# Kernel optimization log

Hardware: AMD Instinct MI355X
Metric: run time of the kernel (lower is better)

The kernel has to match this reference:

```python
import jax, jax.numpy as jnp
import numpy as np

N = 50000   # nodes
E = 400000  # edges
D = 128     # hidden = out dim
H = 4       # heads
DH = 32     # head dim (D // H)
T = 3       # node types
R = 6       # relation (edge) types
L = 2       # layers
EPS = 1e-5


def setup_inputs() -> dict:
    key = jax.random.key(0)
    ks = jax.random.split(key, 12)
    s = D ** -0.5
    sh = DH ** -0.5
    return {
        "h": jax.random.normal(ks[0], (N, D), jnp.float32),
        "src": jax.random.randint(ks[1], (E,), 0, N),
        "dst": jax.random.randint(ks[2], (E,), 0, N),
        "ntype": jnp.sort(jax.random.randint(ks[3], (N,), 0, T)),
        "etype": jnp.sort(jax.random.randint(ks[4], (E,), 0, R)),
        # per-layer HGTConv params (stacked over L)
        "Wk": jax.random.normal(ks[5], (L, T, D, D), jnp.float32) * s,
        "Wq": jax.random.normal(ks[6], (L, T, D, D), jnp.float32) * s,
        "Wv": jax.random.normal(ks[7], (L, T, D, D), jnp.float32) * s,
        "Wa": jax.random.normal(ks[8], (L, T, D, D), jnp.float32) * s,
        "W_att": jax.random.normal(ks[9], (L, H, R, DH, DH), jnp.float32) * sh,
        "W_msg": jax.random.normal(ks[10], (L, H, R, DH, DH), jnp.float32) * sh,
        "pri": jnp.ones((L, H, R), jnp.float32),
        "skip": jnp.ones((L, T), jnp.float32),
        "ln_g": jnp.ones((L, D), jnp.float32),
        "ln_b": jnp.zeros((L, D), jnp.float32),
        # LayerAggregator params
        "agg_w": jnp.ones((L,), jnp.float32),
        "agg_g": jnp.ones((D,), jnp.float32),
        "agg_b": jnp.zeros((D,), jnp.float32),
    }


def typed_linear(x, types, W):
    # W: [T, in, out]; per-node-type linear (DGL TypedLinear, no bias)
    out = x @ W[0]
    for t in range(1, W.shape[0]):
        out = jnp.where((types == t)[:, None], x @ W[t], out)
    return out


def edge_typed(x, etype, W):
    # x: [E, H, DH]; W: [H, R, DH, DH]; per-relation, per-head linear
    out = jnp.einsum('ehd,hdo->eho', x, W[:, 0])
    for r in range(1, W.shape[1]):
        out = jnp.where((etype == r)[:, None, None],
                        jnp.einsum('ehd,hdo->eho', x, W[:, r]), out)
    return out


def layer_norm(x, g, b):
    mu = x.mean(-1, keepdims=True)
    var = ((x - mu) ** 2).mean(-1, keepdims=True)
    return (x - mu) * jax.lax.rsqrt(var + EPS) * g + b


def hgt_layer(x, src, dst, ntype, etype, Wk, Wq, Wv, Wa, W_att, W_msg, pri, skip):
    n = x.shape[0]
    k = typed_linear(x, ntype, Wk).reshape(n, H, DH)
    q = typed_linear(x, ntype, Wq).reshape(n, H, DH)
    v = typed_linear(x, ntype, Wv).reshape(n, H, DH)
    kw = edge_typed(k[src], etype, W_att)          # [E,H,DH]
    mv = edge_typed(v[src], etype, W_msg)          # [E,H,DH]
    a = (kw * q[dst]).sum(-1) * pri.T[etype] / np.sqrt(DH).astype(np.float32)  # [E,H]
    # edge softmax over destination nodes
    mx = jax.lax.stop_gradient(jax.ops.segment_max(a, dst, num_segments=n))
    ex = jnp.exp(a - mx[dst])
    den = jax.ops.segment_sum(ex, dst, num_segments=n)
    att = ex / den[dst]                             # [E,H]
    agg = jax.ops.segment_sum(att[:, :, None] * mv, dst, num_segments=n)
    h_a = typed_linear(agg.reshape(n, H * DH), ntype, Wa)
    sk = jax.nn.sigmoid(skip)[ntype][:, None]
    return h_a * sk + x * (1.0 - sk)                # skip gate (dropout = eval identity)


def reference(h, src, dst, ntype, etype, Wk, Wq, Wv, Wa, W_att, W_msg,
              pri, skip, ln_g, ln_b, agg_w, agg_g, agg_b):
    x = h
    outs = []
    for l in range(L):
        ho = hgt_layer(x, src, dst, ntype, etype, Wk[l], Wq[l], Wv[l], Wa[l],
                       W_att[l], W_msg[l], pri[l], skip[l])
        # residual is Identity (in_dim == out_dim), dropout is eval-mode identity
        x = layer_norm(x + ho, ln_g[l], ln_b[l])
        outs.append(x)
    w = jax.nn.softmax(agg_w)
    mixed = sum(w[i] * outs[i] for i in range(L))
    return layer_norm(mixed, agg_g, agg_b)  # [N, D]; per-type dict is just slicing by ntype
```

## Files before the change

kernel.cpp:

```cpp
#include <hip/hip_runtime.h>

#define NN 50000
#define NE 400000
#define DD 128
#define HH 4
#define DHH 32
#define TT 3
#define RR 6
#define LL 2
#define EPSF 1e-5f

typedef unsigned short ushort_t;
typedef unsigned int uint_t;
typedef __attribute__((ext_vector_type(8))) short short8_t;
typedef __attribute__((ext_vector_type(4))) float float4_t;

__device__ inline ushort_t f2bf(float f){
  union { float f; uint_t u; } x; x.f = f;
  uint_t r = x.u + 0x7fffu + ((x.u >> 16) & 1u);
  return (ushort_t)(r >> 16);
}
__device__ inline float bf2f(ushort_t u){
  union { uint_t u; float f; } x; x.u = ((uint_t)u) << 16;
  return x.f;
}
__device__ inline uint_t pack2(float a, float b){
  return (uint_t)f2bf(a) | ((uint_t)f2bf(b) << 16);
}

__global__ void hist_kernel(const int* __restrict__ dst, int* __restrict__ cnt){
  int e = blockIdx.x*256 + threadIdx.x;
  if (e < NE) atomicAdd(&cnt[dst[e]], 1);
}

__global__ void scan_kernel(const int* __restrict__ deg, int* __restrict__ rowptr){
  __shared__ int wsum[16];
  __shared__ int carrySh;
  int tid = threadIdx.x, lane = tid & 63, w = tid >> 6;
  if (tid == 0){ carrySh = 0; rowptr[0] = 0; }
  __syncthreads();
  for (int base = 0; base < NN; base += 1024){
    int i = base + tid;
    int v = (i < NN) ? deg[i] : 0;
    int s = v;
    #pragma unroll
    for (int off=1; off<64; off<<=1){ int t = __shfl_up(s, off); if (lane >= off) s += t; }
    if (lane == 63) wsum[w] = s;
    __syncthreads();
    if (w == 0 && lane < 16){
      int t = wsum[lane];
      #pragma unroll
      for (int off=1; off<16; off<<=1){ int u = __shfl_up(t, off); if (lane >= off) t += u; }
      wsum[lane] = t;
    }
    __syncthreads();
    int waveOff = (w == 0) ? 0 : wsum[w-1];
    int incl = s + waveOff + carrySh;
    if (i < NN) rowptr[i+1] = incl;
    __syncthreads();
    if (tid == 0) carrySh += wsum[15];
    __syncthreads();
  }
}

__global__ void scatter_kernel(const int* __restrict__ dst, const int* __restrict__ src,
                               const int* __restrict__ etype, const int* __restrict__ rowptr,
                               int* __restrict__ cnt, uint_t* __restrict__ sr){
  int e = blockIdx.x*256 + threadIdx.x;
  if (e < NE){
    int d = dst[e];
    int pos = rowptr[d] + atomicAdd(&cnt[d], 1);
    sr[pos] = (uint_t)src[e] | ((uint_t)etype[e] << 27);
  }
}

__global__ void wprep_kernel(const float* __restrict__ Wk, const float* __restrict__ Wq,
                             const float* __restrict__ Wv, const float* __restrict__ Wa,
                             ushort_t* __restrict__ Wkf, ushort_t* __restrict__ Wqf,
                             ushort_t* __restrict__ Wvf, ushort_t* __restrict__ Waf){
  int i = blockIdx.x*256 + threadIdx.x;
  if (i < TT*DD*DD){
    int j = i & 7, m = (i>>3)&15, kg = (i>>7)&3, ks = (i>>9)&3, tile = (i>>11)&7, t = i>>14;
    int d = ks*32 + kg*4 + (j&3) + ((j>>2)<<4);
    int o = tile*16 + m;
    size_t srcI = (size_t)t*16384 + (size_t)d*DD + o;
    Wkf[i] = f2bf(Wk[srcI]);
    Wqf[i] = f2bf(Wq[srcI]);
    Wvf[i] = f2bf(Wv[srcI]);
    Waf[i] = f2bf(Wa[srcI]);
  }
}

__global__ void wprep2_kernel(const float* __restrict__ Watt, const float* __restrict__ Wmsg,
                              ushort_t* __restrict__ Wattf, ushort_t* __restrict__ Wmsgf){
  int i = blockIdx.x*256 + threadIdx.x;
  if (i < HH*RR*DHH*DHH){
    int j = i & 7, m = (i>>3)&15, kg = (i>>7)&3;
    int tile = (i>>9) % 12, h = i / 6144;
    int nout = tile*16 + m;
    int r = nout >> 5, dd = nout & 31;
    int k = kg*4 + (j&3) + ((j>>2)<<4);
    Wattf[i] = f2bf(Watt[(((h*RR + r)*DHH + dd)<<5) + k]);
    Wmsgf[i] = f2bf(Wmsg[(((h*RR + r)*DHH + k)<<5) + dd]);
  }
}

__global__ __launch_bounds__(256) void kqv_kernel(
    const float* __restrict__ x, const int* __restrict__ ntype,
    const float* __restrict__ Wk, const float* __restrict__ Wq, const float* __restrict__ Wv,
    const ushort_t* __restrict__ Wkf, const ushort_t* __restrict__ Wqf, const ushort_t* __restrict__ Wvf,
    const ushort_t* __restrict__ Wattf, const ushort_t* __restrict__ Wmsgf,
    const float* __restrict__ pri,
    ushort_t* __restrict__ kout, ushort_t* __restrict__ qh, ushort_t* __restrict__ vhat)
{
  __shared__ int nts[16];
  __shared__ ushort_t smem[24704];
  ushort_t* xs_ = smem;
  ushort_t* qs_ = smem + 2112;
  ushort_t* vs_ = smem + 4224;
  ushort_t* ks_ = smem + 6336;
  ushort_t* stg1 = smem;
  ushort_t* stg2 = smem + 12352;
  int tid = threadIdx.x;
  int n0 = blockIdx.x * 16;
  if (tid < 16) nts[tid] = ntype[n0 + tid];
  #pragma unroll
  for (int it=0; it<8; it++){
    int i = tid + it*256;
    xs_[(i>>7)*132 + (i&127)] = f2bf(x[(size_t)n0*DD + i]);
  }
  __syncthreads();
  int t0 = nts[0];
  bool uni = true;
  #pragma unroll
  for (int j=1;j<16;j++) uni = uni && (nts[j] == t0);

  int lane = tid & 63;
  union U8 { struct { uint2 lo, hi; } u; short8_t s; uint4 q; };

  if (uni){
    int w = tid >> 6;
    int m = lane & 15, kg = lane >> 4;
    float4_t acck0{0.f,0.f,0.f,0.f}, acck1{0.f,0.f,0.f,0.f};
    float4_t accq0{0.f,0.f,0.f,0.f}, accq1{0.f,0.f,0.f,0.f};
    float4_t accv0{0.f,0.f,0.f,0.f}, accv1{0.f,0.f,0.f,0.f};
    const ushort_t* wkf = Wkf + (size_t)t0*16384;
    const ushort_t* wqf = Wqf + (size_t)t0*16384;
    const ushort_t* wvf = Wvf + (size_t)t0*16384;
    int tA = 2*w, tB = 2*w+1;
    #pragma unroll
    for (int ks=0; ks<4; ks++){
      U8 a_;
      a_.u.lo = *(const uint2*)&xs_[m*132 + ks*32 + kg*4];
      a_.u.hi = *(const uint2*)&xs_[m*132 + ks*32 + kg*4 + 16];
      int offA = (((tA*4 + ks)*4 + kg) << 7) + (m << 3);
      int offB = (((tB*4 + ks)*4 + kg) << 7) + (m << 3);
      U8 bk0, bk1, bq0, bq1, bv0, bv1;
      bk0.q = *(const uint4*)(wkf + offA);
      bk1.q = *(const uint4*)(wkf + offB);
      bq0.q = *(const uint4*)(wqf + offA);
      bq1.q = *(const uint4*)(wqf + offB);
      bv0.q = *(const uint4*)(wvf + offA);
      bv1.q = *(const uint4*)(wvf + offB);
      acck0 = __builtin_amdgcn_mfma_f32_16x16x32_bf16(bk0.s, a_.s, acck0, 0,0,0);
      acck1 = __builtin_amdgcn_mfma_f32_16x16x32_bf16(bk1.s, a_.s, acck1, 0,0,0);
      accq0 = __builtin_amdgcn_mfma_f32_16x16x32_bf16(bq0.s, a_.s, accq0, 0,0,0);
      accq1 = __builtin_amdgcn_mfma_f32_16x16x32_bf16(bq1.s, a_.s, accq1, 0,0,0);
      accv0 = __builtin_amdgcn_mfma_f32_16x16x32_bf16(bv0.s, a_.s, accv0, 0,0,0);
      accv1 = __builtin_amdgcn_mfma_f32_16x16x32_bf16(bv1.s, a_.s, accv1, 0,0,0);
    }
    int cA = tA*16 + (kg<<2), cB = tB*16 + (kg<<2);
    *(uint2*)(&ks_[m*132 + cA]) = make_uint2(pack2(acck0[0],acck0[1]), pack2(acck0[2],acck0[3]));
    *(uint2*)(&ks_[m*132 + cB]) = make_uint2(pack2(acck1[0],acck1[1]), pack2(acck1[2],acck1[3]));
    *(uint2*)(&qs_[m*132 + cA]) = make_uint2(pack2(accq0[0],accq0[1]), pack2(accq0[2],accq0[3]));
    *(uint2*)(&qs_[m*132 + cB]) = make_uint2(pack2(accq1[0],accq1[1]), pack2(accq1[2],accq1[3]));
    *(uint2*)(&vs_[m*132 + cA]) = make_uint2(pack2(accv0[0],accv0[1]), pack2(accv0[2],accv0[3]));
    *(uint2*)(&vs_[m*132 + cB]) = make_uint2(pack2(accv1[0],accv1[1]), pack2(accv1[2],accv1[3]));
  } else {
    int c = tid & 127, nb = (tid >> 7) * 8;
    float ak[8], aq[8], av[8];
    #pragma unroll
    for (int j=0;j<8;j++){ ak[j]=0.f; aq[j]=0.f; av[j]=0.f; }
    #pragma unroll
    for (int j=0;j<8;j++){
      int t = nts[nb+j];
      const float* wk = Wk + (size_t)t*DD*DD + c;
      const float* wq = Wq + (size_t)t*DD*DD + c;
      const float* wv = Wv + (size_t)t*DD*DD + c;
      float sk=0.f, sq=0.f, sv=0.f;
      for (int d=0; d<DD; d++){
        float xv = bf2f(xs_[(nb+j)*132 + d]);
        sk += xv*wk[d*DD];
        sq += xv*wq[d*DD];
        sv += xv*wv[d*DD];
      }
      ak[j]=sk; aq[j]=sq; av[j]=sv;
    }
    #pragma unroll
    for (int j=0;j<8;j++){
      ks_[(nb+j)*132 + c]=f2bf(ak[j]);
      qs_[(nb+j)*132 + c]=f2bf(aq[j]);
      vs_[(nb+j)*132 + c]=f2bf(av[j]);
    }
  }
  __syncthreads();

  int h = tid >> 6;
  int m = lane & 15, kg = lane >> 4;
  U8 aq_, av_;
  aq_.u.lo = *(const uint2*)&qs_[m*132 + (h<<5) + (kg<<2)];
  aq_.u.hi = *(const uint2*)&qs_[m*132 + (h<<5) + (kg<<2) + 16];
  av_.u.lo = *(const uint2*)&vs_[m*132 + (h<<5) + (kg<<2)];
  av_.u.hi = *(const uint2*)&vs_[m*132 + (h<<5) + (kg<<2) + 16];
  {
    int row = tid >> 4, coff = (tid & 15) * 8;
    uint4 kv4;
    kv4.x = *(const uint_t*)&ks_[row*132 + coff];
    kv4.y = *(const uint_t*)&ks_[row*132 + coff + 2];
    kv4.z = *(const uint_t*)&ks_[row*132 + coff + 4];
    kv4.w = *(const uint_t*)&ks_[row*132 + coff + 6];
    *(uint4*)(kout + (size_t)(n0+row)*DD + coff) = kv4;
  }
  __syncthreads();

  const ushort_t* wqb = Wattf + h*(RR*DHH*DHH);
  const ushort_t* wvb = Wmsgf + h*(RR*DHH*DHH);

  #pragma unroll
  for (int nt=0; nt<12; nt++){
    int frag = ((nt*4 + kg)<<7) + (m<<3);
    U8 bq_;
    bq_.q = *(const uint4*)(wqb + frag);
    float4_t accq{0.f,0.f,0.f,0.f};
    accq = __builtin_amdgcn_mfma_f32_16x16x32_bf16(bq_.s, aq_.s, accq, 0,0,0);
    int nout0 = nt*16 + (kg<<2);
    int r = nout0 >> 5, dd0 = nout0 & 31;
    float scale = pri[h*RR + r] * 0.17677669529663687f;
    *(uint2*)(&stg1[m*772 + r*DD + (h<<5) + dd0]) =
        make_uint2(pack2(accq[0]*scale, accq[1]*scale), pack2(accq[2]*scale, accq[3]*scale));
  }
  __syncthreads();

  #pragma unroll
  for (int it=0; it<6; it++){
    int idx = tid + it*256;
    int row = idx / 96;
    int off = (idx - row*96) * 8;
    uint4 q4;
    q4.x = *(const uint_t*)&stg1[row*772 + off];
    q4.y = *(const uint_t*)&stg1[row*772 + off + 2];
    q4.z = *(const uint_t*)&stg1[row*772 + off + 4];
    q4.w = *(const uint_t*)&stg1[row*772 + off + 6];
    *(uint4*)(qh + (size_t)(n0+row)*768 + off) = q4;
  }
  #pragma unroll
  for (int nt=0; nt<12; nt++){
    int frag = ((nt*4 + kg)<<7) + (m<<3);
    U8 bv_;
    bv_.q = *(const uint4*)(wvb + frag);
    float4_t accv{0.f,0.f,0.f,0.f};
    accv = __builtin_amdgcn_mfma_f32_16x16x32_bf16(bv_.s, av_.s, accv, 0,0,0);
    int nout0 = nt*16 + (kg<<2);
    int r = nout0 >> 5, dd0 = nout0 & 31;
    *(uint2*)(&stg2[m*772 + r*DD + (h<<5) + dd0]) =
        make_uint2(pack2(accv[0],accv[1]), pack2(accv[2],accv[3]));
  }
  __syncthreads();

  #pragma unroll
  for (int it=0; it<6; it++){
    int idx = tid + it*256;
    int row = idx / 96;
    int off = (idx - row*96) * 8;
    uint4 v4;
    v4.x = *(const uint_t*)&stg2[row*772 + off];
    v4.y = *(const uint_t*)&stg2[row*772 + off + 2];
    v4.z = *(const uint_t*)&stg2[row*772 + off + 4];
    v4.w = *(const uint_t*)&stg2[row*772 + off + 6];
    *(uint4*)(vhat + (size_t)(n0+row)*768 + off) = v4;
  }
}

__global__ __launch_bounds__(256) void reduce_kernel(
    const ushort_t* __restrict__ kb, const ushort_t* __restrict__ qh,
    const ushort_t* __restrict__ vhat,
    const int* __restrict__ rowptr, const uint_t* __restrict__ src_r,
    ushort_t* __restrict__ agg16)
{
  int n = blockIdx.x*4 + (threadIdx.x >> 6);
  if (n >= NN) return;
  int lane = threadIdx.x & 63;
  int b = rowptr[n], e1 = rowptr[n+1];
  const uint_t* qbase = (const uint_t*)(qh + (size_t)n*RR*DD) + lane;
  uint_t qn0 = qbase[0*64], qn1 = qbase[1*64], qn2 = qbase[2*64];
  uint_t qn3 = qbase[3*64], qn4 = qbase[4*64], qn5 = qbase[5*64];
  float m = -1e30f, den = 0.f, ac0 = 0.f, ac1 = 0.f;
  for (int i=b; i<e1; i+=8){
    int m8 = e1 - i; if (m8 > 8) m8 = 8;
    uint_t sr8[8];
    #pragma unroll
    for (int jj=0;jj<8;jj++) sr8[jj] = src_r[i + ((jj < m8) ? jj : (m8-1))];
    uint_t kk8[8], vv8[8];
    #pragma unroll
    for (int jj=0;jj<8;jj++){
      uint_t sr_ = sr8[jj];
      size_t s = (size_t)(sr_ & 0x07FFFFFFu);
      kk8[jj] = *(const uint_t*)(kb + s*DD + (lane<<1));
      vv8[jj] = *(const uint_t*)(vhat + (s*RR + (sr_>>27))*DD + (lane<<1));
    }
    float p8[8];
    #pragma unroll
    for (int jj=0;jj<8;jj++){
      int r = (int)(sr8[jj] >> 27);
      uint_t qw = qn0;
      qw = (r==1) ? qn1 : qw;
      qw = (r==2) ? qn2 : qw;
      qw = (r==3) ? qn3 : qw;
      qw = (r==4) ? qn4 : qw;
      qw = (r==5) ? qn5 : qw;
      uint_t kw = kk8[jj];
      float pp = bf2f((ushort_t)(kw & 0xffffu))*bf2f((ushort_t)(qw & 0xffffu))
               + bf2f((ushort_t)(kw >> 16))   *bf2f((ushort_t)(qw >> 16));
      #pragma unroll
      for (int off=1; off<16; off<<=1) pp += __shfl_xor(pp, off);
      p8[jj] = (jj < m8) ? pp : -1e30f;
    }
    float mb = p8[0];
    #pragma unroll
    for (int jj=1;jj<8;jj++) mb = fmaxf(mb, p8[jj]);
    float mnew = fmaxf(m, mb);
    float corr = __expf(m - mnew);
    den *= corr; ac0 *= corr; ac1 *= corr;
    m = mnew;
    #pragma unroll
    for (int jj=0;jj<8;jj++){
      float ex = __expf(p8[jj] - m);
      den += ex;
      ac0 += ex * bf2f((ushort_t)(vv8[jj] & 0xffffu));
      ac1 += ex * bf2f((ushort_t)(vv8[jj] >> 16));
    }
  }
  float inv = (den > 0.f) ? 1.f/den : 0.f;
  uint_t packed = (uint_t)f2bf(ac0*inv) | ((uint_t)f2bf(ac1*inv) << 16);
  *(uint_t*)(agg16 + (size_t)n*DD + (lane<<1)) = packed;
}

__global__ __launch_bounds__(256) void ha_kernel(
    const ushort_t* __restrict__ agg16, const float* __restrict__ x, const int* __restrict__ ntype,
    const float* __restrict__ Wa, const ushort_t* __restrict__ Waf, const float* __restrict__ skipl,
    const float* __restrict__ lng, const float* __restrict__ lnb,
    float* __restrict__ xout)
{
  __shared__ ushort_t as[16][132];
  __shared__ float xs[16][132];
  __shared__ int nts[16];
  int tid = threadIdx.x;
  int n0 = blockIdx.x * 16;
  {
    int row = tid >> 4, col = (tid & 15) * 8;
    uint4 t4 = *(const uint4*)(agg16 + (size_t)(n0+row)*DD + col);
    *(uint2*)&as[row][col]   = make_uint2(t4.x, t4.y);
    *(uint2*)&as[row][col+4] = make_uint2(t4.z, t4.w);
  }
  if (tid < 16) nts[tid] = ntype[n0 + tid];
  __syncthreads();
  int t0 = nts[0];
  bool uni = true;
  #pragma unroll
  for (int j=1;j<16;j++) uni = uni && (nts[j] == t0);

  if (uni){
    int lane = tid & 63, w = tid >> 6;
    int m = lane & 15, kg = lane >> 4;
    float4_t acc0{0.f,0.f,0.f,0.f}, acc1{0.f,0.f,0.f,0.f};
    const ushort_t* waf = Waf + (size_t)t0*16384;
    int tA = 2*w, tB = 2*w+1;
    union U8 { struct { uint2 lo, hi; } u; short8_t s; uint4 q; };
    #pragma unroll
    for (int ks=0; ks<4; ks++){
      U8 a_;
      a_.u.lo = *(const uint2*)&as[m][ks*32 + kg*4];
      a_.u.hi = *(const uint2*)&as[m][ks*32 + kg*4 + 16];
      U8 b0, b1;
      b0.q = *(const uint4*)(waf + ((((tA*4 + ks)*4 + kg) << 7) + (m << 3)));
      b1.q = *(const uint4*)(waf + ((((tB*4 + ks)*4 + kg) << 7) + (m << 3)));
      acc0 = __builtin_amdgcn_mfma_f32_16x16x32_bf16(b0.s, a_.s, acc0, 0,0,0);
      acc1 = __builtin_amdgcn_mfma_f32_16x16x32_bf16(b1.s, a_.s, acc1, 0,0,0);
    }
    float sk = 1.f/(1.f + __expf(-skipl[t0]));
    int cA = tA*16 + (kg<<2), cB = tB*16 + (kg<<2);
    #pragma unroll
    for (int i=0;i<4;i++){
      float xva = x[(size_t)(n0+m)*DD + cA + i];
      float xvb = x[(size_t)(n0+m)*DD + cB + i];
      xs[m][cA+i] = acc0[i]*sk + xva*(2.f - sk);
      xs[m][cB+i] = acc1[i]*sk + xvb*(2.f - sk);
    }
  } else {
    int c = tid & 127, nb = (tid >> 7) * 8;
    float acc[8];
    #pragma unroll
    for (int j=0;j<8;j++) acc[j]=0.f;
    #pragma unroll
    for (int j=0;j<8;j++){
      int t = nts[nb+j];
      const float* wa = Wa + (size_t)t*DD*DD + c;
      float sacc2 = 0.f;
      for (int d=0; d<DD; d++)
        sacc2 += bf2f(as[nb+j][d]) * wa[d*DD];
      acc[j] = sacc2;
    }
    #pragma unroll
    for (int j=0;j<8;j++){
      int n = n0 + nb + j;
      float sk2 = 1.f/(1.f + __expf(-skipl[nts[nb+j]]));
      float xv = x[(size_t)n*DD + c];
      xs[nb+j][c] = acc[j]*sk2 + xv*(2.f - sk2);
    }
  }
  __syncthreads();
  int lane = tid & 63;
  int r0 = tid >> 6;
  #pragma unroll
  for (int rr = r0; rr < 16; rr += 4){
    float t0v = xs[rr][lane], t1v = xs[rr][lane+64];
    float s = t0v + t1v;
    #pragma unroll
    for (int off=32; off>0; off>>=1) s += __shfl_xor(s, off);
    float mu = s * (1.f/DD);
    float d0 = t0v-mu, d1 = t1v-mu;
    float vs = d0*d0 + d1*d1;
    #pragma unroll
    for (int off=32; off>0; off>>=1) vs += __shfl_xor(vs, off);
    float inv = rsqrtf(vs*(1.f/DD) + EPSF);
    size_t base = (size_t)(n0+rr)*DD;
    xout[base+lane]    = d0*inv*lng[lane]    + lnb[lane];
    xout[base+lane+64] = d1*inv*lng[lane+64] + lnb[lane+64];
  }
}

__global__ __launch_bounds__(256) void final_kernel(
    const float* __restrict__ x1, const float* __restrict__ x2,
    const float* __restrict__ aggw, const float* __restrict__ g, const float* __restrict__ b,
    float* __restrict__ out)
{
  int lane = threadIdx.x & 63;
  int n = blockIdx.x*4 + (threadIdx.x >> 6);
  float a0 = aggw[0], a1 = aggw[1];
  float m = fmaxf(a0, a1);
  float e0 = __expf(a0-m), e1 = __expf(a1-m);
  float inv01 = 1.f/(e0+e1);
  float w0 = e0*inv01, w1 = e1*inv01;
  size_t base = (size_t)n*DD;
  float t0 = w0*x1[base+lane]    + w1*x2[base+lane];
  float t1 = w0*x1[base+lane+64] + w1*x2[base+lane+64];
  float s = t0 + t1;
  #pragma unroll
  for (int off=32; off>0; off>>=1) s += __shfl_xor(s, off);
  float mu = s * (1.f/DD);
  float d0 = t0-mu, d1 = t1-mu;
  float vs = d0*d0 + d1*d1;
  #pragma unroll
  for (int off=32; off>0; off>>=1) vs += __shfl_xor(vs, off);
  float invv = rsqrtf(vs*(1.f/DD) + EPSF);
  out[base+lane]    = d0*invv*g[lane]    + b[lane];
  out[base+lane+64] = d1*invv*g[lane+64] + b[lane+64];
}

extern "C" void kernel_launch(void* const* d_in, const int* in_sizes, int n_in,
                              void* d_out, int out_size, void* d_ws, size_t ws_size,
                              hipStream_t stream)
{
  (void)in_sizes; (void)n_in; (void)out_size; (void)ws_size;
  const float* h_in  = (const float*)d_in[0];
  const int*   src   = (const int*)d_in[1];
  const int*   dst   = (const int*)d_in[2];
  const int*   ntype = (const int*)d_in[3];
  const int*   etype = (const int*)d_in[4];
  const float* Wk    = (const float*)d_in[5];
  const float* Wq    = (const float*)d_in[6];
  const float* Wv    = (const float*)d_in[7];
  const float* Wa    = (const float*)d_in[8];
  const float* Watt  = (const float*)d_in[9];
  const float* Wmsg  = (const float*)d_in[10];
  const float* pri   = (const float*)d_in[11];
  const float* skp   = (const float*)d_in[12];
  const float* lng   = (const float*)d_in[13];
  const float* lnb   = (const float*)d_in[14];
  const float* aggw  = (const float*)d_in[15];
  const float* aggg  = (const float*)d_in[16];
  const float* aggb_ = (const float*)d_in[17];

  size_t P = (size_t)NN*DD;
  ushort_t* kb16 = (ushort_t*)d_ws;
  ushort_t* qh   = kb16 + P;
  ushort_t* vhat = qh + (size_t)NN*RR*DD;
  float* out0  = (float*)(vhat + (size_t)NN*RR*DD);
  int* rowptr = (int*)(out0 + P);
  int* cnt    = rowptr + NN + 1;
  uint_t* srcr = (uint_t*)(cnt + NN);
  ushort_t* wkF = (ushort_t*)(srcr + NE);
  ushort_t* wqF = wkF + (size_t)TT*DD*DD;
  ushort_t* wvF = wqF + (size_t)TT*DD*DD;
  ushort_t* waF = wvF + (size_t)TT*DD*DD;
  ushort_t* wattF = waF + (size_t)TT*DD*DD;
  ushort_t* wmsgF = wattF + (size_t)HH*RR*DHH*DHH;
  ushort_t* agg16 = qh;
  float* xout = (float*)d_out;

  hipMemsetAsync(cnt, 0, NN*sizeof(int), stream);
  hist_kernel<<<(NE+255)/256, 256, 0, stream>>>(dst, cnt);
  scan_kernel<<<1, 1024, 0, stream>>>(cnt, rowptr);
  hipMemsetAsync(cnt, 0, NN*sizeof(int), stream);
  scatter_kernel<<<(NE+255)/256, 256, 0, stream>>>(dst, src, etype, rowptr, cnt, srcr);

  const float* x = h_in;
  for (int l=0; l<LL; l++){
    const float* Wk_l  = Wk  + (size_t)l*TT*DD*DD;
    const float* Wq_l  = Wq  + (size_t)l*TT*DD*DD;
    const float* Wv_l  = Wv  + (size_t)l*TT*DD*DD;
    const float* Wa_l  = Wa  + (size_t)l*TT*DD*DD;
    const float* Wat_l = Watt + (size_t)l*HH*RR*DHH*DHH;
    const float* Wms_l = Wmsg + (size_t)l*HH*RR*DHH*DHH;
    const float* pri_l = pri + (size_t)l*HH*RR;
    const float* skp_l = skp + (size_t)l*TT;

    wprep_kernel<<<(TT*DD*DD+255)/256, 256, 0, stream>>>(Wk_l, Wq_l, Wv_l, Wa_l,
                                                         wkF, wqF, wvF, waF);
    wprep2_kernel<<<(HH*RR*DHH*DHH+255)/256, 256, 0, stream>>>(Wat_l, Wms_l, wattF, wmsgF);
    kqv_kernel<<<NN/16, 256, 0, stream>>>(x, ntype, Wk_l, Wq_l, Wv_l, wkF, wqF, wvF,
                                          wattF, wmsgF, pri_l, kb16, qh, vhat);
    reduce_kernel<<<(NN+3)/4, 256, 0, stream>>>(kb16, qh, vhat, rowptr, srcr, agg16);
    float* xo = (l == 0) ? out0 : xout;
    ha_kernel<<<NN/16, 256, 0, stream>>>(agg16, x, ntype, Wa_l, waF, skp_l,
                                         lng + (size_t)l*DD, lnb + (size_t)l*DD, xo);
    x = xo;
  }
  final_kernel<<<NN/4, 256, 0, stream>>>(out0, xout, aggw, aggg, aggb_, xout);
}
```

Measured before the change: 433.2 us.

## Defer per-relation message transform until after aggregation in reduce kernel

Instead of precomputing V transformed by every relation's W_msg per node (a 6x-wide vhat array) and gathering it per edge, kqv now writes plain V. The reduce kernel accumulates softmax-weighted V separately for each relation type in registers and applies W_msg once per destination node. This removes the 768-wide vhat write and cuts each edge gather from relation-specific rows to a 128-wide row. In exchange it adds 12 accumulators per lane with select logic, a shared-memory staging step, and a per-node fp32 matvec that reads W_msg from global memory.

```diff
diff --git a/kernel.cpp b/kernel.cpp
--- a/kernel.cpp
+++ b/kernel.cpp
@@ -91,8 +91,7 @@
   }
 }
 
-__global__ void wprep2_kernel(const float* __restrict__ Watt, const float* __restrict__ Wmsg,
-                              ushort_t* __restrict__ Wattf, ushort_t* __restrict__ Wmsgf){
+__global__ void wprep2_kernel(const float* __restrict__ Watt, ushort_t* __restrict__ Wattf){
   int i = blockIdx.x*256 + threadIdx.x;
   if (i < HH*RR*DHH*DHH){
     int j = i & 7, m = (i>>3)&15, kg = (i>>7)&3;
@@ -101,7 +100,6 @@
     int r = nout >> 5, dd = nout & 31;
     int k = kg*4 + (j&3) + ((j>>2)<<4);
     Wattf[i] = f2bf(Watt[(((h*RR + r)*DHH + dd)<<5) + k]);
-    Wmsgf[i] = f2bf(Wmsg[(((h*RR + r)*DHH + k)<<5) + dd]);
   }
 }
 
@@ -109,18 +107,16 @@
     const float* __restrict__ x, const int* __restrict__ ntype,
     const float* __restrict__ Wk, const float* __restrict__ Wq, const float* __restrict__ Wv,
     const ushort_t* __restrict__ Wkf, const ushort_t* __restrict__ Wqf, const ushort_t* __restrict__ Wvf,
-    const ushort_t* __restrict__ Wattf, const ushort_t* __restrict__ Wmsgf,
-    const float* __restrict__ pri,
-    ushort_t* __restrict__ kout, ushort_t* __restrict__ qh, ushort_t* __restrict__ vhat)
+    const ushort_t* __restrict__ Wattf, const float* __restrict__ pri,
+    ushort_t* __restrict__ kout, ushort_t* __restrict__ vout, ushort_t* __restrict__ qh)
 {
   __shared__ int nts[16];
-  __shared__ ushort_t smem[24704];
+  __shared__ ushort_t smem[12352];
   ushort_t* xs_ = smem;
   ushort_t* qs_ = smem + 2112;
   ushort_t* vs_ = smem + 4224;
   ushort_t* ks_ = smem + 6336;
-  ushort_t* stg1 = smem;
-  ushort_t* stg2 = smem + 12352;
+  ushort_t* stg = smem;
   int tid = threadIdx.x;
   int n0 = blockIdx.x * 16;
   if (tid < 16) nts[tid] = ntype[n0 + tid];
@@ -207,25 +203,26 @@
 
   int h = tid >> 6;
   int m = lane & 15, kg = lane >> 4;
-  U8 aq_, av_;
+  U8 aq_;
   aq_.u.lo = *(const uint2*)&qs_[m*132 + (h<<5) + (kg<<2)];
   aq_.u.hi = *(const uint2*)&qs_[m*132 + (h<<5) + (kg<<2) + 16];
-  av_.u.lo = *(const uint2*)&vs_[m*132 + (h<<5) + (kg<<2)];
-  av_.u.hi = *(const uint2*)&vs_[m*132 + (h<<5) + (kg<<2) + 16];
   {
     int row = tid >> 4, coff = (tid & 15) * 8;
-    uint4 kv4;
+    uint4 kv4, vv4;
     kv4.x = *(const uint_t*)&ks_[row*132 + coff];
     kv4.y = *(const uint_t*)&ks_[row*132 + coff + 2];
     kv4.z = *(const uint_t*)&ks_[row*132 + coff + 4];
     kv4.w = *(const uint_t*)&ks_[row*132 + coff + 6];
+    vv4.x = *(const uint_t*)&vs_[row*132 + coff];
+    vv4.y = *(const uint_t*)&vs_[row*132 + coff + 2];
+    vv4.z = *(const uint_t*)&vs_[row*132 + coff + 4];
+    vv4.w = *(const uint_t*)&vs_[row*132 + coff + 6];
     *(uint4*)(kout + (size_t)(n0+row)*DD + coff) = kv4;
+    *(uint4*)(vout + (size_t)(n0+row)*DD + coff) = vv4;
   }
   __syncthreads();
 
   const ushort_t* wqb = Wattf + h*(RR*DHH*DHH);
-  const ushort_t* wvb = Wmsgf + h*(RR*DHH*DHH);
-
   #pragma unroll
   for (int nt=0; nt<12; nt++){
     int frag = ((nt*4 + kg)<<7) + (m<<3);
@@ -236,65 +233,41 @@
     int nout0 = nt*16 + (kg<<2);
     int r = nout0 >> 5, dd0 = nout0 & 31;
     float scale = pri[h*RR + r] * 0.17677669529663687f;
-    *(uint2*)(&stg1[m*772 + r*DD + (h<<5) + dd0]) =
+    *(uint2*)(&stg[m*772 + r*DD + (h<<5) + dd0]) =
         make_uint2(pack2(accq[0]*scale, accq[1]*scale), pack2(accq[2]*scale, accq[3]*scale));
   }
   __syncthreads();
-
   #pragma unroll
   for (int it=0; it<6; it++){
     int idx = tid + it*256;
     int row = idx / 96;
     int off = (idx - row*96) * 8;
     uint4 q4;
-    q4.x = *(const uint_t*)&stg1[row*772 + off];
-    q4.y = *(const uint_t*)&stg1[row*772 + off + 2];
-    q4.z = *(const uint_t*)&stg1[row*772 + off + 4];
-    q4.w = *(const uint_t*)&stg1[row*772 + off + 6];
+    q4.x = *(const uint_t*)&stg[row*772 + off];
+    q4.y = *(const uint_t*)&stg[row*772 + off + 2];
+    q4.z = *(const uint_t*)&stg[row*772 + off + 4];
+    q4.w = *(const uint_t*)&stg[row*772 + off + 6];
     *(uint4*)(qh + (size_t)(n0+row)*768 + off) = q4;
   }
-  #pragma unroll
-  for (int nt=0; nt<12; nt++){
-    int frag = ((nt*4 + kg)<<7) + (m<<3);
-    U8 bv_;
-    bv_.q = *(const uint4*)(wvb + frag);
-    float4_t accv{0.f,0.f,0.f,0.f};
-    accv = __builtin_amdgcn_mfma_f32_16x16x32_bf16(bv_.s, av_.s, accv, 0,0,0);
-    int nout0 = nt*16 + (kg<<2);
-    int r = nout0 >> 5, dd0 = nout0 & 31;
-    *(uint2*)(&stg2[m*772 + r*DD + (h<<5) + dd0]) =
-        make_uint2(pack2(accv[0],accv[1]), pack2(accv[2],accv[3]));
-  }
-  __syncthreads();
-
-  #pragma unroll
-  for (int it=0; it<6; it++){
-    int idx = tid + it*256;
-    int row = idx / 96;
-    int off = (idx - row*96) * 8;
-    uint4 v4;
-    v4.x = *(const uint_t*)&stg2[row*772 + off];
-    v4.y = *(const uint_t*)&stg2[row*772 + off + 2];
-    v4.z = *(const uint_t*)&stg2[row*772 + off + 4];
-    v4.w = *(const uint_t*)&stg2[row*772 + off + 6];
-    *(uint4*)(vhat + (size_t)(n0+row)*768 + off) = v4;
-  }
 }
 
 __global__ __launch_bounds__(256) void reduce_kernel(
-    const ushort_t* __restrict__ kb, const ushort_t* __restrict__ qh,
-    const ushort_t* __restrict__ vhat,
+    const ushort_t* __restrict__ kb, const ushort_t* __restrict__ vb,
+    const ushort_t* __restrict__ qh, const float* __restrict__ Wmsg,
     const int* __restrict__ rowptr, const uint_t* __restrict__ src_r,
     ushort_t* __restrict__ agg16)
 {
-  int n = blockIdx.x*4 + (threadIdx.x >> 6);
-  if (n >= NN) return;
+  __shared__ float sacc_s[4][RR][DD];
+  int wid = threadIdx.x >> 6;
+  int n = blockIdx.x*4 + wid;
   int lane = threadIdx.x & 63;
   int b = rowptr[n], e1 = rowptr[n+1];
   const uint_t* qbase = (const uint_t*)(qh + (size_t)n*RR*DD) + lane;
   uint_t qn0 = qbase[0*64], qn1 = qbase[1*64], qn2 = qbase[2*64];
   uint_t qn3 = qbase[3*64], qn4 = qbase[4*64], qn5 = qbase[5*64];
-  float m = -1e30f, den = 0.f, ac0 = 0.f, ac1 = 0.f;
+  float m = -1e30f, den = 0.f;
+  float a00=0.f,a01=0.f,a10=0.f,a11=0.f,a20=0.f,a21=0.f;
+  float a30=0.f,a31=0.f,a40=0.f,a41=0.f,a50=0.f,a51=0.f;
   for (int i=b; i<e1; i+=8){
     int m8 = e1 - i; if (m8 > 8) m8 = 8;
     uint_t sr8[8];
@@ -306,7 +279,7 @@
       uint_t sr_ = sr8[jj];
       size_t s = (size_t)(sr_ & 0x07FFFFFFu);
       kk8[jj] = *(const uint_t*)(kb + s*DD + (lane<<1));
-      vv8[jj] = *(const uint_t*)(vhat + (s*RR + (sr_>>27))*DD + (lane<<1));
+      vv8[jj] = *(const uint_t*)(vb + s*DD + (lane<<1));
     }
     float p8[8];
     #pragma unroll
@@ -330,19 +303,49 @@
     for (int jj=1;jj<8;jj++) mb = fmaxf(mb, p8[jj]);
     float mnew = fmaxf(m, mb);
     float corr = __expf(m - mnew);
-    den *= corr; ac0 *= corr; ac1 *= corr;
+    den *= corr;
+    a00*=corr; a01*=corr; a10*=corr; a11*=corr; a20*=corr; a21*=corr;
+    a30*=corr; a31*=corr; a40*=corr; a41*=corr; a50*=corr; a51*=corr;
     m = mnew;
     #pragma unroll
     for (int jj=0;jj<8;jj++){
       float ex = __expf(p8[jj] - m);
       den += ex;
-      ac0 += ex * bf2f((ushort_t)(vv8[jj] & 0xffffu));
-      ac1 += ex * bf2f((ushort_t)(vv8[jj] >> 16));
+      float v0 = ex * bf2f((ushort_t)(vv8[jj] & 0xffffu));
+      float v1 = ex * bf2f((ushort_t)(vv8[jj] >> 16));
+      int r = (int)(sr8[jj] >> 27);
+      a00 += (r==0)?v0:0.f; a01 += (r==0)?v1:0.f;
+      a10 += (r==1)?v0:0.f; a11 += (r==1)?v1:0.f;
+      a20 += (r==2)?v0:0.f; a21 += (r==2)?v1:0.f;
+      a30 += (r==3)?v0:0.f; a31 += (r==3)?v1:0.f;
+      a40 += (r==4)?v0:0.f; a41 += (r==4)?v1:0.f;
+      a50 += (r==5)?v0:0.f; a51 += (r==5)?v1:0.f;
     }
   }
   float inv = (den > 0.f) ? 1.f/den : 0.f;
-  uint_t packed = (uint_t)f2bf(ac0*inv) | ((uint_t)f2bf(ac1*inv) << 16);
-  *(uint_t*)(agg16 + (size_t)n*DD + (lane<<1)) = packed;
+  int d0 = lane << 1;
+  sacc_s[wid][0][d0] = a00*inv; sacc_s[wid][0][d0+1] = a01*inv;
+  sacc_s[wid][1][d0] = a10*inv; sacc_s[wid][1][d0+1] = a11*inv;
+  sacc_s[wid][2][d0] = a20*inv; sacc_s[wid][2][d0+1] = a21*inv;
+  sacc_s[wid][3][d0] = a30*inv; sacc_s[wid][3][d0+1] = a31*inv;
+  sacc_s[wid][4][d0] = a40*inv; sacc_s[wid][4][d0+1] = a41*inv;
+  sacc_s[wid][5][d0] = a50*inv; sacc_s[wid][5][d0+1] = a51*inv;
+  __syncthreads();
+  int h = lane >> 4;
+  int o2 = (lane & 15) << 1;
+  float m0 = 0.f, m1 = 0.f;
+  #pragma unroll
+  for (int r=0;r<RR;r++){
+    const float* wm = Wmsg + ((h*RR + r) << 10);
+    const float* sa = &sacc_s[wid][r][h<<5];
+    #pragma unroll 8
+    for (int d=0; d<DHH; d++){
+      float sv = sa[d];
+      float2 w2 = *(const float2*)(wm + (d<<5) + o2);
+      m0 += sv*w2.x; m1 += sv*w2.y;
+    }
+  }
+  *(uint_t*)(agg16 + (size_t)n*DD + d0) = pack2(m0, m1);
 }
 
 __global__ __launch_bounds__(256) void ha_kernel(
@@ -493,9 +496,10 @@
 
   size_t P = (size_t)NN*DD;
   ushort_t* kb16 = (ushort_t*)d_ws;
-  ushort_t* qh   = kb16 + P;
-  ushort_t* vhat = qh + (size_t)NN*RR*DD;
-  float* out0  = (float*)(vhat + (size_t)NN*RR*DD);
+  ushort_t* vb16 = kb16 + P;
+  ushort_t* qh   = vb16 + P;
+  ushort_t* agg16 = qh + (size_t)NN*RR*DD;
+  float* out0  = (float*)(agg16 + P);
   int* rowptr = (int*)(out0 + P);
   int* cnt    = rowptr + NN + 1;
   uint_t* srcr = (uint_t*)(cnt + NN);
@@ -504,8 +508,6 @@
   ushort_t* wvF = wqF + (size_t)TT*DD*DD;
   ushort_t* waF = wvF + (size_t)TT*DD*DD;
   ushort_t* wattF = waF + (size_t)TT*DD*DD;
-  ushort_t* wmsgF = wattF + (size_t)HH*RR*DHH*DHH;
-  ushort_t* agg16 = qh;
   float* xout = (float*)d_out;
 
   hipMemsetAsync(cnt, 0, NN*sizeof(int), stream);
@@ -527,10 +529,10 @@
 
     wprep_kernel<<<(TT*DD*DD+255)/256, 256, 0, stream>>>(Wk_l, Wq_l, Wv_l, Wa_l,
                                                          wkF, wqF, wvF, waF);
-    wprep2_kernel<<<(HH*RR*DHH*DHH+255)/256, 256, 0, stream>>>(Wat_l, Wms_l, wattF, wmsgF);
+    wprep2_kernel<<<(HH*RR*DHH*DHH+255)/256, 256, 0, stream>>>(Wat_l, wattF);
     kqv_kernel<<<NN/16, 256, 0, stream>>>(x, ntype, Wk_l, Wq_l, Wv_l, wkF, wqF, wvF,
-                                          wattF, wmsgF, pri_l, kb16, qh, vhat);
-    reduce_kernel<<<(NN+3)/4, 256, 0, stream>>>(kb16, qh, vhat, rowptr, srcr, agg16);
+                                          wattF, pri_l, kb16, vb16, qh);
+    reduce_kernel<<<NN/4, 256, 0, stream>>>(kb16, vb16, qh, Wms_l, rowptr, srcr, agg16);
     float* xo = (l == 0) ? out0 : xout;
     ha_kernel<<<NN/16, 256, 0, stream>>>(agg16, x, ntype, Wa_l, waF, skp_l,
                                          lng + (size_t)l*DD, lnb + (size_t)l*DD, xo);
```

New measurement: 960.4 us. 2.22x slower.
